# Optimization experiments

Measured on AMD Instinct MI355X. Metric: run time of the kernel, lower is better.

Reference implementation:

```python
import jax, jax.numpy as jnp
import numpy as np

IN_F, OUT_F, GROUP = 4096, 11008, 128
N_GROUPS = IN_F // GROUP  # 32 (in_features divisible by group_size -> no padding)


def setup_inputs() -> dict:
    key = jax.random.key(0)
    kx, kw, ks, kb = jax.random.split(key, 4)
    x = jax.random.normal(kx, (4, 2048, IN_F), dtype=jnp.float32)
    weight_q = jax.random.randint(kw, (OUT_F, IN_F), -128, 128, dtype=jnp.int32).astype(jnp.int8)
    scales = jax.random.uniform(ks, (OUT_F, N_GROUPS), dtype=jnp.float32) * 0.01 + 1e-4
    bias = jax.random.normal(kb, (OUT_F,), dtype=jnp.float32)
    return {"x": x, "weight_q": weight_q, "scales": scales, "bias": bias}


def reference(x, weight_q, scales, bias):
    # Dequantize: group-wise scale along in_features, cast to fp16 (as torch .half())
    W = (weight_q.astype(jnp.float32).reshape(OUT_F, N_GROUPS, GROUP)
         * scales[:, :, None]).reshape(OUT_F, IN_F).astype(jnp.float16)
    # fp16 linear: y = x W^T + b, then back to fp32
    y = jnp.einsum('bsi,oi->bso', x.astype(jnp.float16), W) + bias.astype(jnp.float16)
    return y.astype(jnp.float32)
```

## Files before the change

### kernel.cpp

```cpp
#include <hip/hip_runtime.h>

#define IN_F 4096
#define OUT_F 11008
#define NGROUPS 32
#define M_TOTAL 8192
#define BM 256
#define BN 256
#define BK 64
#define NKT (IN_F / BK)

typedef _Float16 half_t;
typedef __attribute__((ext_vector_type(8))) _Float16 half8;
typedef __attribute__((ext_vector_type(4))) _Float16 half4v;
typedef __attribute__((ext_vector_type(4))) float f32x4;
typedef __attribute__((ext_vector_type(4))) int i32x4;

typedef __attribute__((address_space(1))) const void gvoid_t;
typedef __attribute__((address_space(3))) void lvoid_t;

__global__ void convert_x_k(const float* __restrict__ x, half_t* __restrict__ xh) {
  const int n4 = M_TOTAL * IN_F / 4;
  int stride = gridDim.x * blockDim.x;
  for (int i = blockIdx.x * blockDim.x + threadIdx.x; i < n4; i += stride) {
    f32x4 v = __builtin_nontemporal_load((const f32x4*)x + i);
    half4v h;
    h[0] = (_Float16)v[0]; h[1] = (_Float16)v[1];
    h[2] = (_Float16)v[2]; h[3] = (_Float16)v[3];
    ((half4v*)xh)[i] = h;
  }
}

__global__ void dequant_w_k(const int* __restrict__ wq,
                            const float* __restrict__ scales,
                            half_t* __restrict__ wh) {
  int row = blockIdx.x;
  int t = threadIdx.x;
  size_t base = (size_t)row * IN_F + (size_t)t * 8;
  float s = scales[row * NGROUPS + (t >> 4)];
  i32x4 q0 = __builtin_nontemporal_load((const i32x4*)(wq + base));
  i32x4 q1 = __builtin_nontemporal_load((const i32x4*)(wq + base) + 1);
  half8 h;
#pragma unroll
  for (int j = 0; j < 4; ++j) h[j] = (_Float16)((float)q0[j] * s);
#pragma unroll
  for (int j = 0; j < 4; ++j) h[4 + j] = (_Float16)((float)q1[j] * s);
  *(half8*)(wh + base) = h;
}


__device__ __forceinline__ void rd4(half8 (&d)[4], const char* base) {
#pragma unroll
  for (int i = 0; i < 4; ++i) d[i] = *(const half8*)(base + i * 1024);
}

__device__ __forceinline__ void mfma16(f32x4 (&acc)[8][4], const half8 (&a)[4],
                                       const half8 (&b)[4], int mh) {
#pragma unroll
  for (int i = 0; i < 4; ++i)
#pragma unroll
    for (int j = 0; j < 4; ++j)
      acc[mh * 4 + i][j] =
          __builtin_amdgcn_mfma_f32_16x16x32_f16(a[i], b[j], acc[mh * 4 + i][j], 0, 0, 0);
}

#define BAR() __builtin_amdgcn_s_barrier()
#define SB0() __builtin_amdgcn_sched_barrier(0)
#define PRIO1() __builtin_amdgcn_s_setprio(1)
#define PRIO0() __builtin_amdgcn_s_setprio(0)
#define VMCNT(N) asm volatile("s_waitcnt vmcnt(" #N ")" ::: "memory")
#define LGKM(N) asm volatile("s_waitcnt lgkmcnt(" #N ")" ::: "memory")

#define STAGE(OP, KH, KT, S)                                                          \
  do {                                                                                \
    const half_t* g_ = ((OP) ? pBsrc : pAsrc) + (KT) * 64 + (KH) * 32;                \
    char* d_ = (char*)&lds[S][OP][KH][0] + wvoff;                                     \
    __builtin_amdgcn_global_load_lds((gvoid_t*)g_, (lvoid_t*)d_, 16, 0, 0);           \
    __builtin_amdgcn_global_load_lds((gvoid_t*)(g_ + 128 * IN_F),                     \
                                     (lvoid_t*)(d_ + 8192), 16, 0, 0);                \
  } while (0)

#define PH(SL, KH, MH, RB, SOP, SKH, SKT, SSL, FENCE)                  \
  do {                                                                 \
    rd4(a, (const char*)&lds[SL][0][KH][0] + aoff + (MH) * 4096);      \
    if (RB) rd4(b, (const char*)&lds[SL][1][KH][0] + boff);            \
    STAGE(SOP, SKH, SKT, SSL);                                         \
    SB0(); BAR();                                                      \
    LGKM(0); SB0(); PRIO1();                                           \
    mfma16(acc, a, b, MH);                                             \
    PRIO0();                                                           \
    if (FENCE) VMCNT(6);                                               \
    BAR(); SB0();                                                      \
  } while (0)

#define PHN(SL, KH, MH, RB, FENCE)                                     \
  do {                                                                 \
    rd4(a, (const char*)&lds[SL][0][KH][0] + aoff + (MH) * 4096);      \
    if (RB) rd4(b, (const char*)&lds[SL][1][KH][0] + boff);            \
    SB0(); BAR();                                                      \
    LGKM(0); SB0(); PRIO1();                                           \
    mfma16(acc, a, b, MH);                                             \
    PRIO0();                                                           \
    if (FENCE) VMCNT(0);                                               \
    BAR(); SB0();                                                      \
  } while (0)

__global__ __launch_bounds__(512, 1) void gemm_k(const half_t* __restrict__ A,
                                                 const half_t* __restrict__ B,
                                                 const float* __restrict__ bias,
                                                 float* __restrict__ C) {
  __shared__ __align__(16) half_t lds[2][2][2][8192];

  const int tid = threadIdx.x;
  const int lane = tid & 63;
  const int wv = tid >> 6;
  const int wm = wv >> 2;
  const int wn = wv & 3;
  const int wvoff = wv << 10;

  const int nwg = gridDim.x;
  const int perx = nwg >> 3;
  const int L = ((int)blockIdx.x & 7) * perx + ((int)blockIdx.x >> 3);
  const int band = L >> 7;
  const int rr_ = L & 127;
  const int bn0 = band << 2;
  const int cols = (43 - bn0) < 4 ? (43 - bn0) : 4;
  const int bm = rr_ / cols;
  const int bn = bn0 + rr_ % cols;
  const int row0 = bm * BM;
  const int col0 = bn * BN;

  const int c16 = (tid & 3) * 16;
  const int srow = tid >> 2;
  const int clog = c16 ^ ((srow & 6) << 3);
  const int kidx = clog >> 1;
  const half_t* pAsrc = A + (size_t)(row0 + srow) * IN_F + kidx;
  const half_t* pBsrc = B + (size_t)(col0 + srow) * IN_F + kidx;

  const int r16 = lane & 15;
  const int kg = lane >> 4;
  const int arow = wm * 128 + r16;
  const int brow = wn * 64 + r16;
  const int aoff = arow * 64 + ((kg * 16) ^ ((arow & 6) << 3));
  const int boff = brow * 64 + ((kg * 16) ^ ((brow & 6) << 3));

  f32x4 acc[8][4];
#pragma unroll
  for (int m = 0; m < 8; ++m)
#pragma unroll
    for (int n = 0; n < 4; ++n) acc[m][n] = (f32x4){0.f, 0.f, 0.f, 0.f};

  STAGE(0, 0, 0, 0);
  STAGE(1, 0, 0, 0);
  STAGE(0, 1, 0, 0);
  STAGE(1, 1, 0, 0);
  STAGE(0, 0, 1, 1);
  STAGE(1, 0, 1, 1);
  STAGE(1, 1, 1, 1);
  VMCNT(6);
  BAR();
  SB0();

  half8 a[4], b[4];
  for (int u = 0; u < 31; ++u) {
    const int t1 = 2 * u + 1, n0 = 2 * u + 2, n1 = 2 * u + 3;
    PH(0, 0, 0, 1, 0, 1, t1, 1, 0);
    PH(0, 0, 1, 0, 1, 0, n0, 0, 0);
    PH(0, 1, 0, 1, 0, 0, n0, 0, 0);
    PH(0, 1, 1, 0, 1, 1, n0, 0, 1);
    PH(1, 0, 0, 1, 0, 1, n0, 0, 0);
    PH(1, 0, 1, 0, 1, 0, n1, 1, 0);
    PH(1, 1, 0, 1, 0, 0, n1, 1, 0);
    PH(1, 1, 1, 0, 1, 1, n1, 1, 1);
  }
  {
    PH(0, 0, 0, 1, 0, 1, 63, 1, 0);
    PHN(0, 0, 1, 0, 0);
    PHN(0, 1, 0, 1, 0);
    PHN(0, 1, 1, 0, 2);
    PHN(1, 0, 0, 1, 0);
    PHN(1, 0, 1, 0, 0);
    PHN(1, 1, 0, 1, 0);
    PHN(1, 1, 1, 0, 0);
  }

  const int kg4 = kg * 4;
#pragma unroll
  for (int nf = 0; nf < 4; ++nf) {
    int col = col0 + wn * 64 + nf * 16 + r16;
    _Float16 bh = (_Float16)bias[col];
#pragma unroll
    for (int mf = 0; mf < 8; ++mf) {
      int rb = row0 + wm * 128 + mf * 16 + kg4;
#pragma unroll
      for (int r = 0; r < 4; ++r) {
        _Float16 v = (_Float16)acc[mf][nf][r] + bh;
        __builtin_nontemporal_store((float)v, &C[(size_t)(rb + r) * OUT_F + col]);
      }
    }
  }
}

__global__ void naive_k(const float* __restrict__ x, const int* __restrict__ wq,
                        const float* __restrict__ scales, const float* __restrict__ bias,
                        float* __restrict__ out) {
  long idx = (long)blockIdx.x * blockDim.x + threadIdx.x;
  if (idx >= (long)M_TOTAL * OUT_F) return;
  int m = (int)(idx / OUT_F);
  int n = (int)(idx % OUT_F);
  float acc = 0.f;
  for (int g = 0; g < NGROUPS; ++g) {
    float s = scales[n * NGROUPS + g];
    for (int k = g * 128; k < (g + 1) * 128; ++k) {
      _Float16 xv = (_Float16)x[(size_t)m * IN_F + k];
      _Float16 wv = (_Float16)((float)wq[(size_t)n * IN_F + k] * s);
      acc += (float)xv * (float)wv;
    }
  }
  _Float16 r = (_Float16)acc + (_Float16)bias[n];
  out[idx] = (float)r;
}

extern "C" void kernel_launch(void* const* d_in, const int* in_sizes, int n_in,
                              void* d_out, int out_size, void* d_ws, size_t ws_size,
                              hipStream_t stream) {
  const float* x = (const float*)d_in[0];
  const int* wq = (const int*)d_in[1];
  const float* scales = (const float*)d_in[2];
  const float* bias = (const float*)d_in[3];
  float* out = (float*)d_out;

  const size_t xh_bytes = (size_t)M_TOTAL * IN_F * sizeof(half_t);
  const size_t wh_bytes = (size_t)OUT_F * IN_F * sizeof(half_t);

  if (ws_size >= xh_bytes + wh_bytes) {
    half_t* xh = (half_t*)d_ws;
    half_t* wh = (half_t*)((char*)d_ws + xh_bytes);
    convert_x_k<<<2048, 256, 0, stream>>>(x, xh);
    dequant_w_k<<<OUT_F, 512, 0, stream>>>(wq, scales, wh);
    gemm_k<<<(M_TOTAL / BM) * (OUT_F / BN), 512, 0, stream>>>(xh, wh, bias, out);
  } else {
    long total = (long)M_TOTAL * OUT_F;
    naive_k<<<(int)((total + 255) / 256), 256, 0, stream>>>(x, wq, scales, bias, out);
  }
}
```

Baseline: 775.5 us.

## Merge GEMM phases to halve barriers and issue two stage loads per phase

Restructures the main GEMM loop from eight half-tile phases per iteration into four phases. Each phase reads both A halves and B from LDS, issues two global-to-LDS stage loads and runs both MFMA halves. This halves the number of barrier and wait pairs per K step, cutting synchronization overhead. In exchange it holds more fragment registers (a0, a1, b) and changes the prefetch depth and vmcnt fences, which shifts how load latency overlaps with compute.

```diff
diff --git a/kernel.cpp b/kernel.cpp
--- a/kernel.cpp
+++ b/kernel.cpp
@@ -79,29 +79,35 @@
                                      (lvoid_t*)(d_ + 8192), 16, 0, 0);                \
   } while (0)
 
-#define PH(SL, KH, MH, RB, SOP, SKH, SKT, SSL, FENCE)                  \
-  do {                                                                 \
-    rd4(a, (const char*)&lds[SL][0][KH][0] + aoff + (MH) * 4096);      \
-    if (RB) rd4(b, (const char*)&lds[SL][1][KH][0] + boff);            \
-    STAGE(SOP, SKH, SKT, SSL);                                         \
-    SB0(); BAR();                                                      \
-    LGKM(0); SB0(); PRIO1();                                           \
-    mfma16(acc, a, b, MH);                                             \
-    PRIO0();                                                           \
-    if (FENCE) VMCNT(6);                                               \
-    BAR(); SB0();                                                      \
+#define MPH(SL, KH, S1OP, S1KT, S1SL, S1KH, S2OP, S2KT, S2SL, S2KH, FENCE)   \
+  do {                                                                       \
+    rd4(a0, (const char*)&lds[SL][0][KH][0] + aoff);                         \
+    rd4(a1, (const char*)&lds[SL][0][KH][0] + aoff + 4096);                  \
+    rd4(b, (const char*)&lds[SL][1][KH][0] + boff);                          \
+    STAGE(S1OP, S1KH, S1KT, S1SL);                                           \
+    STAGE(S2OP, S2KH, S2KT, S2SL);                                           \
+    SB0(); BAR();                                                            \
+    LGKM(0); SB0(); PRIO1();                                                 \
+    mfma16(acc, a0, b, 0);                                                   \
+    mfma16(acc, a1, b, 1);                                                   \
+    PRIO0();                                                                 \
+    if ((FENCE) == 8) VMCNT(8);                                              \
+    BAR(); SB0();                                                            \
   } while (0)
 
-#define PHN(SL, KH, MH, RB, FENCE)                                     \
-  do {                                                                 \
-    rd4(a, (const char*)&lds[SL][0][KH][0] + aoff + (MH) * 4096);      \
-    if (RB) rd4(b, (const char*)&lds[SL][1][KH][0] + boff);            \
-    SB0(); BAR();                                                      \
-    LGKM(0); SB0(); PRIO1();                                           \
-    mfma16(acc, a, b, MH);                                             \
-    PRIO0();                                                           \
-    if (FENCE) VMCNT(0);                                               \
-    BAR(); SB0();                                                      \
+#define MPHN(SL, KH, FENCE)                                                  \
+  do {                                                                       \
+    rd4(a0, (const char*)&lds[SL][0][KH][0] + aoff);                         \
+    rd4(a1, (const char*)&lds[SL][0][KH][0] + aoff + 4096);                  \
+    rd4(b, (const char*)&lds[SL][1][KH][0] + boff);                          \
+    SB0(); BAR();                                                            \
+    LGKM(0); SB0(); PRIO1();                                                 \
+    mfma16(acc, a0, b, 0);                                                   \
+    mfma16(acc, a1, b, 1);                                                   \
+    PRIO0();                                                                 \
+    if ((FENCE) == 4) VMCNT(4);                                              \
+    if ((FENCE) == 0) VMCNT(0);                                              \
+    BAR(); SB0();                                                            \
   } while (0)
 
 __global__ __launch_bounds__(512, 1) void gemm_k(const half_t* __restrict__ A,
@@ -155,32 +161,23 @@
   STAGE(1, 1, 0, 0);
   STAGE(0, 0, 1, 1);
   STAGE(1, 0, 1, 1);
-  STAGE(1, 1, 1, 1);
-  VMCNT(6);
+  VMCNT(4);
   BAR();
   SB0();
 
-  half8 a[4], b[4];
+  half8 a0[4], a1[4], b[4];
   for (int u = 0; u < 31; ++u) {
     const int t1 = 2 * u + 1, n0 = 2 * u + 2, n1 = 2 * u + 3;
-    PH(0, 0, 0, 1, 0, 1, t1, 1, 0);
-    PH(0, 0, 1, 0, 1, 0, n0, 0, 0);
-    PH(0, 1, 0, 1, 0, 0, n0, 0, 0);
-    PH(0, 1, 1, 0, 1, 1, n0, 0, 1);
-    PH(1, 0, 0, 1, 0, 1, n0, 0, 0);
-    PH(1, 0, 1, 0, 1, 0, n1, 1, 0);
-    PH(1, 1, 0, 1, 0, 0, n1, 1, 0);
-    PH(1, 1, 1, 0, 1, 1, n1, 1, 1);
+    MPH(0, 0, 0, t1, 1, 1, 1, t1, 1, 1, 8);
+    MPH(0, 1, 0, n0, 0, 0, 1, n0, 0, 0, 8);
+    MPH(1, 0, 0, n0, 0, 1, 1, n0, 0, 1, 8);
+    MPH(1, 1, 0, n1, 1, 0, 1, n1, 1, 0, 8);
   }
   {
-    PH(0, 0, 0, 1, 0, 1, 63, 1, 0);
-    PHN(0, 0, 1, 0, 0);
-    PHN(0, 1, 0, 1, 0);
-    PHN(0, 1, 1, 0, 2);
-    PHN(1, 0, 0, 1, 0);
-    PHN(1, 0, 1, 0, 0);
-    PHN(1, 1, 0, 1, 0);
-    PHN(1, 1, 1, 0, 0);
+    MPH(0, 0, 0, 63, 1, 1, 1, 63, 1, 1, 8);
+    MPHN(0, 1, 4);
+    MPHN(1, 0, 0);
+    MPHN(1, 1, -1);
   }
 
   const int kg4 = kg * 4;
```

Measured after the change: 786.8 us. No clear change (+1.5%).
